# Kernel tuning notes

Hardware: AMD Instinct MI355X
Metric: run time of the kernel (lower is better)

The kernel has to match this reference:

```python
import jax, jax.numpy as jnp
import numpy as np

WINDOW = 5
D_CONV = 4
HEADDIM = 64
NGROUPS = 1
EPS = 1e-5


def _silu(x):
    return x * jax.nn.sigmoid(x)


def _causal_dwconv(x, w, b):
    # x: (B, L, C), w: (C, K), b: (C,) -- depthwise causal conv along L
    K = w.shape[1]
    L = x.shape[1]
    xp = jnp.pad(x, ((0, 0), (K - 1, 0), (0, 0)))
    y = b
    for k in range(K):
        y = y + xp[:, k:k + L, :] * w[:, k]
    return y


def _mamba2_layer(x, in_w, cw, cb, dtb, A_log, Dh, nw, ow):
    # x: (B, L, dim). Mamba2 mixer (mamba_ssm defaults: ngroups=1, rmsnorm gated, no proj bias)
    B, L, _ = x.shape
    d_inner = nw.shape[0]
    nheads = dtb.shape[0]
    p = d_inner // nheads
    conv_dim = cw.shape[0]
    n = (conv_dim - d_inner) // 2  # d_state
    zxbcdt = x @ in_w.T  # (B, L, 2*d_inner + 2*n + nheads)
    z, xBC, dt = jnp.split(zxbcdt, [d_inner, d_inner + conv_dim], axis=-1)
    dt = jax.nn.softplus(dt + dtb)  # (B, L, h)
    xBC = _silu(_causal_dwconv(xBC, cw, cb))
    xh, Bm, Cm = jnp.split(xBC, [d_inner, d_inner + n], axis=-1)
    xh = xh.reshape(B, L, nheads, p)
    A = -jnp.exp(A_log)  # (h,)

    def step(h, inp):
        dt_t, x_t, B_t, C_t = inp  # (B,h), (B,h,p), (B,n), (B,n)
        decay = jnp.exp(dt_t * A)  # (B,h)
        h = h * decay[..., None, None] + (dt_t[..., None] * x_t)[..., None] * B_t[:, None, None, :]
        y = jnp.einsum('bhpn,bn->bhp', h, C_t)
        return h, y

    h0 = jnp.zeros((B, nheads, p, n), x.dtype)
    _, ys = jax.lax.scan(step, h0, (dt.transpose(1, 0, 2), xh.transpose(1, 0, 2, 3),
                                    Bm.transpose(1, 0, 2), Cm.transpose(1, 0, 2)))
    y = ys.transpose(1, 0, 2, 3) + Dh[None, None, :, None] * xh  # (B, L, h, p)
    y = y.reshape(B, L, d_inner)
    # gated RMSNorm (norm_before_gate=False): gate then normalize
    y = y * _silu(z)
    y = y * jax.lax.rsqrt(jnp.mean(y * y, axis=-1, keepdims=True) + EPS) * nw
    return y @ ow.T


def setup_inputs() -> dict:
    key = jax.random.key(0)
    ks = iter(jax.random.split(key, 24))
    B, T, C = 8, 2048, 3
    dim, depth, d_state, expand = 128, 4, 64, 2
    d_inner = expand * dim
    nheads = d_inner // HEADDIM
    conv_dim = d_inner + 2 * NGROUPS * d_state
    d_in_proj = 2 * d_inner + 2 * NGROUPS * d_state + nheads
    nrm = lambda shp, s=1.0: jax.random.normal(next(ks), shp, jnp.float32) * s
    return {
        'x': nrm((B, T, C)),
        'mlp_w1': nrm((128, C * WINDOW), 0.2), 'mlp_b1': jnp.zeros((128,), jnp.float32),
        'mlp_w2': nrm((dim, 128), 0.1), 'mlp_b2': jnp.zeros((dim,), jnp.float32),
        'cls_token': nrm((1, 1, dim)),
        'in_proj_w': nrm((depth, d_in_proj, dim), 0.05),
        'conv_w': nrm((depth, conv_dim, D_CONV), 0.3),
        'conv_b': jnp.zeros((depth, conv_dim), jnp.float32),
        'dt_bias': nrm((depth, nheads), 0.5),
        'A_log': jnp.log(jax.random.uniform(next(ks), (depth, nheads), jnp.float32, 1.0, 16.0)),
        'Dh': jnp.ones((depth, nheads), jnp.float32),
        'norm_w': jnp.ones((depth, d_inner), jnp.float32),
        'out_proj_w': nrm((depth, dim, d_inner), 0.05),
        'ln_w': jnp.ones((dim,), jnp.float32), 'ln_b': jnp.zeros((dim,), jnp.float32),
        'head_w': nrm((1, dim), 0.1), 'head_b': jnp.zeros((1,), jnp.float32),
    }


def reference(x, mlp_w1, mlp_b1, mlp_w2, mlp_b2, cls_token, in_proj_w, conv_w, conv_b,
              dt_bias, A_log, Dh, norm_w, out_proj_w, ln_w, ln_b, head_w, head_b):
    B, T, C = x.shape
    L = T - WINDOW + 1
    # Unfold + rearrange 'b (c w) l -> b l (w c)' == sliding windows flattened (window outer, channel inner)
    tok = jnp.stack([x[:, k:k + L, :] for k in range(WINDOW)], axis=2).reshape(B, L, WINDOW * C)
    h = jax.nn.gelu(tok @ mlp_w1.T + mlp_b1, approximate=False) @ mlp_w2.T + mlp_b2
    dim = h.shape[-1]
    h = jnp.concatenate([h, jnp.broadcast_to(cls_token, (B, 1, dim))], axis=1)
    for i in range(in_proj_w.shape[0]):
        h = _mamba2_layer(h, in_proj_w[i], conv_w[i], conv_b[i], dt_bias[i],
                          A_log[i], Dh[i], norm_w[i], out_proj_w[i])
    cls = h[:, -1]
    mu = jnp.mean(cls, axis=-1, keepdims=True)
    var = jnp.mean((cls - mu) ** 2, axis=-1, keepdims=True)
    cls_n = (cls - mu) * jax.lax.rsqrt(var + 1e-5) * ln_w + ln_b
    out = (cls_n @ head_w.T + head_b)[:, 0]
    return out, h
```

## Files before the change

### kernel.cpp

```cpp
#include <hip/hip_runtime.h>
#include <math.h>

#define BATCH 8
#define TSEQ 2048
#define CIN 3
#define WIN 5
#define LSEQ 2044
#define LH 2045
#define LHP 2048
#define DIM 128
#define DEPTH 4
#define DIN 256
#define NH 4
#define PDIM 64
#define NSTATE 64
#define CONVD 384
#define DPROJ 644
#define NJT 41
#define QC 64
#define NCH 32
#define LDS2 68
#define LDSY 268
#define LDSH 140
#define FTR 32
#define OTOK 32

typedef __attribute__((ext_vector_type(8))) short bf16x8;
typedef __attribute__((ext_vector_type(4))) float f32x4;
union Frag8 { bf16x8 v; uint2 u[2]; };

__device__ __forceinline__ float sigmoidf_(float x){ return 1.f/(1.f+__expf(-x)); }
__device__ __forceinline__ float siluf_(float x){ return x*sigmoidf_(x); }
__device__ __forceinline__ unsigned short f2bf(float f){
  unsigned int u = __float_as_uint(f);
  return (unsigned short)((u + 0x7FFFu + ((u >> 16) & 1u)) >> 16);
}
__device__ __forceinline__ float bf2f(unsigned short u){
  return __uint_as_float(((unsigned int)u) << 16);
}
__device__ __forceinline__ unsigned int pack2(float a, float b){
  return (unsigned int)f2bf(a) | ((unsigned int)f2bf(b) << 16);
}
__device__ __forceinline__ unsigned int pack2lo(float a, float b){
  float ra = a - bf2f(f2bf(a)), rb = b - bf2f(f2bf(b));
  return (unsigned int)f2bf(ra) | ((unsigned int)f2bf(rb) << 16);
}
__device__ __forceinline__ bf16x8 ldfrag(const unsigned short* base, int off){
  Frag8 f;
  f.u[0] = *(const uint2*)(base + off);
  f.u[1] = *(const uint2*)(base + off + 4);
  return f.v;
}

__global__ void __launch_bounds__(256) k_cast_all(
    const float* __restrict__ w, const float* __restrict__ ow,
    const float* __restrict__ cls,
    unsigned short* __restrict__ wH, unsigned short* __restrict__ wL,
    unsigned short* __restrict__ oH, unsigned short* __restrict__ oL,
    unsigned short* __restrict__ hH, unsigned short* __restrict__ hL) {
  int blk = blockIdx.x;
  if (blk < 164) {
    int gid = blk*256 + threadIdx.x;
    int lane = gid & 63;
    int kb = (gid >> 6) & 3;
    int jt = (gid >> 8) % NJT;
    int ly = gid / (NJT*4*64);
    int m = lane & 15, q = lane >> 4;
    int j = jt*16 + m;
    int k = kb*32 + q*8;
    unsigned short hi[8], lo[8];
    if (j < DPROJ) {
      const float* src = w + ((size_t)ly*DPROJ + j)*DIM + k;
#pragma unroll
      for (int i = 0; i < 8; ++i) {
        float v = src[i];
        hi[i] = f2bf(v);
        lo[i] = f2bf(v - bf2f(hi[i]));
      }
    } else {
#pragma unroll
      for (int i = 0; i < 8; ++i) { hi[i] = 0; lo[i] = 0; }
    }
    size_t dst = (size_t)gid*8;
    *(uint4*)(wH + dst) = *(const uint4*)hi;
    *(uint4*)(wL + dst) = *(const uint4*)lo;
  } else if (blk < 228) {
    int gid = (blk - 164)*256 + threadIdx.x;
    int lane = gid & 63;
    int kb = (gid >> 6) & 7;
    int jt = (gid >> 9) & 7;
    int ly = gid >> 12;
    int m = lane & 15, q = lane >> 4;
    int j = jt*16 + m;
    int k = kb*32 + q*8;
    const float* src = ow + ((size_t)ly*DIM + j)*DIN + k;
    unsigned short hi[8], lo[8];
#pragma unroll
    for (int i = 0; i < 8; ++i) {
      float v = src[i];
      hi[i] = f2bf(v);
      lo[i] = f2bf(v - bf2f(hi[i]));
    }
    size_t dst = (size_t)gid*8;
    *(uint4*)(oH + dst) = *(const uint4*)hi;
    *(uint4*)(oL + dst) = *(const uint4*)lo;
  } else {
    int t = threadIdx.x;
    if (t < DIM) {
      float cv = cls[t];
      unsigned short hi = f2bf(cv);
      unsigned short lo = f2bf(cv - bf2f(hi));
      for (int b = 0; b < BATCH; ++b) {
        hH[((size_t)b*LHP + LSEQ)*DIM + t] = hi;
        hL[((size_t)b*LHP + LSEQ)*DIM + t] = lo;
      }
    }
  }
}

__global__ void __launch_bounds__(512) k_front(
    const float* __restrict__ x, const float* __restrict__ w1,
    const float* __restrict__ b1, const float* __restrict__ w2,
    const float* __restrict__ b2,
    unsigned short* __restrict__ hH, unsigned short* __restrict__ hL) {
  int t = threadIdx.x;
  int b = blockIdx.x >> 6;
  int c0 = (blockIdx.x & 63) * FTR;
  __shared__ float xs[(FTR+4)*CIN];
  __shared__ float w1s[DIM*17];
  __shared__ __align__(16) float h1s[FTR][DIM];
  __shared__ float part[FTR][DIM][2];
  for (int i = t; i < (FTR+4)*CIN; i += 512) {
    int row = c0 + i/3, ch = i - (i/3)*3;
    xs[i] = (row < TSEQ) ? x[(size_t)b*TSEQ*CIN + (size_t)row*CIN + ch] : 0.f;
  }
  for (int i = t; i < DIM*15; i += 512) {
    int j = i/15, k = i - j*15;
    w1s[j*17+k] = w1[i];
  }
  __syncthreads();
  {
    int j = t & 127, rh = t >> 7;
    float bias = b1[j];
    const float* wr = &w1s[j*17];
    for (int r = rh*8; r < rh*8+8; ++r) {
      float a = bias;
#pragma unroll
      for (int k = 0; k < 15; ++k) a += xs[r*3+k]*wr[k];
      h1s[r][j] = 0.5f*a*(1.f + erff(a*0.70710678118654752f));
    }
  }
  __syncthreads();
  {
    int j = t & 127, z = t >> 7;
    int hf = z & 1, rh2 = z >> 1;
    float4 wv[16];
    const float4* w2r = (const float4*)(w2 + (size_t)j*DIM + hf*64);
#pragma unroll
    for (int k4 = 0; k4 < 16; ++k4) wv[k4] = w2r[k4];
#pragma unroll 2
    for (int r = rh2*16; r < rh2*16+16; ++r) {
      const float4* hr = (const float4*)&h1s[r][hf*64];
      float acc = 0.f;
#pragma unroll
      for (int k4 = 0; k4 < 16; ++k4) {
        float4 hv = hr[k4];
        acc += wv[k4].x*hv.x + wv[k4].y*hv.y + wv[k4].z*hv.z + wv[k4].w*hv.w;
      }
      part[r][j][hf] = acc;
    }
  }
  __syncthreads();
  {
    int c = t & 127, rh = t >> 7;
    float bias = b2[c];
    for (int r = rh*8; r < rh*8+8; ++r) {
      int l = c0 + r;
      if (l < LSEQ) {
        float val = part[r][c][0] + part[r][c][1] + bias;
        unsigned short hi = f2bf(val);
        hH[((size_t)b*LHP + l)*DIM + c] = hi;
        hL[((size_t)b*LHP + l)*DIM + c] = f2bf(val - bf2f(hi));
      }
    }
  }
}

__global__ void __launch_bounds__(256) k_inproj_mfma(
    const unsigned short* __restrict__ hH, const unsigned short* __restrict__ hL,
    const unsigned short* __restrict__ wH, const unsigned short* __restrict__ wL,
    const float* __restrict__ dtb, float* __restrict__ zx) {
  int b = blockIdx.x >> 6;
  int r = blockIdx.x & 63;
  int lb = r >> 1, jh = r & 1;
  int wv = threadIdx.x >> 6, lane = threadIdx.x & 63;
  int l0 = lb*64 + wv*16;
  int m = lane & 15, q = lane >> 4;
  size_t hoff = ((size_t)b*LHP + (l0 + m))*DIM + q*8;
  bf16x8 ah[4], al[4];
#pragma unroll
  for (int kb = 0; kb < 4; ++kb) {
    ah[kb] = *(const bf16x8*)(hH + hoff + kb*32);
    al[kb] = *(const bf16x8*)(hL + hoff + kb*32);
  }
  int jt0 = jh ? 21 : 0, jtn = jh ? NJT : 21;
#pragma unroll 2
  for (int jt = jt0; jt < jtn; ++jt) {
    size_t woff = (((size_t)jt*4)*64 + lane)*8;
    bf16x8 bh[4], bl[4];
#pragma unroll
    for (int kb = 0; kb < 4; ++kb) {
      bh[kb] = *(const bf16x8*)(wH + woff + (size_t)kb*64*8);
      bl[kb] = *(const bf16x8*)(wL + woff + (size_t)kb*64*8);
    }
    f32x4 acc = {0.f, 0.f, 0.f, 0.f};
#pragma unroll
    for (int kb = 0; kb < 4; ++kb)
      acc = __builtin_amdgcn_mfma_f32_16x16x32_bf16(al[kb], bh[kb], acc, 0, 0, 0);
#pragma unroll
    for (int kb = 0; kb < 4; ++kb)
      acc = __builtin_amdgcn_mfma_f32_16x16x32_bf16(ah[kb], bl[kb], acc, 0, 0, 0);
#pragma unroll
    for (int kb = 0; kb < 4; ++kb)
      acc = __builtin_amdgcn_mfma_f32_16x16x32_bf16(ah[kb], bh[kb], acc, 0, 0, 0);
    int jj = jt*16 + m;
    if (jj < DPROJ) {
      bool isdt = (jj >= 640);
      float bias = isdt ? dtb[jj - 640] : 0.f;
#pragma unroll
      for (int rr = 0; rr < 4; ++rr) {
        int tok = l0 + q*4 + rr;
        if (tok < LH) {
          float v = acc[rr];
          if (isdt) { v += bias; v = (v > 20.f) ? v : log1pf(__expf(v)); }
          zx[((size_t)b*LH + tok)*DPROJ + jj] = v;
        }
      }
    }
  }
}

__global__ void k_conv(const float* __restrict__ zx, const float* __restrict__ cw,
                       const float* __restrict__ cb, float* __restrict__ xbc) {
  size_t idx = (size_t)blockIdx.x*blockDim.x + threadIdx.x;
  const size_t total = (size_t)BATCH*LH*(CONVD/4);
  if (idx >= total) return;
  int c4 = (int)(idx % (CONVD/4)) * 4;
  size_t bl = idx / (CONVD/4);
  int l = (int)(bl % LH); int b = (int)(bl / LH);
  float4 w0 = *(const float4*)(cw + (c4+0)*4);
  float4 w1 = *(const float4*)(cw + (c4+1)*4);
  float4 w2 = *(const float4*)(cw + (c4+2)*4);
  float4 w3 = *(const float4*)(cw + (c4+3)*4);
  float4 a = *(const float4*)(cb + c4);
#pragma unroll
  for (int k = 0; k < 4; ++k) {
    int tin = l - 3 + k;
    if (tin >= 0) {
      float4 v = *(const float4*)(zx + ((size_t)b*LH + tin)*DPROJ + DIN + c4);
      a.x += v.x * ((const float*)&w0)[k];
      a.y += v.y * ((const float*)&w1)[k];
      a.z += v.z * ((const float*)&w2)[k];
      a.w += v.w * ((const float*)&w3)[k];
    }
  }
  float4 o;
  o.x = siluf_(a.x); o.y = siluf_(a.y); o.z = siluf_(a.z); o.w = siluf_(a.w);
  *(float4*)(xbc + ((size_t)b*LH + l)*CONVD + c4) = o;
}

__global__ void __launch_bounds__(256, 4) k_chunk_state(
    const float* __restrict__ zx, const float* __restrict__ xbc,
    const float* __restrict__ A_log, float* __restrict__ G, float* __restrict__ dec) {
  int blk = blockIdx.x;
  int c = blk & (NCH-1), hd = (blk >> 5) & 3, b = blk >> 7;
  int t0 = c*QC;
  int tid = threadIdx.x;
  int wv = tid >> 6, lane = tid & 63;
  int m = lane & 15, q = lane >> 4;
  float A = -__expf(A_log[hd]);
  __shared__ __align__(16) unsigned short BcH[QC*LDS2], BcL[QC*LDS2];
  __shared__ __align__(16) unsigned short XtH[QC*LDS2], XtL[QC*LDS2];
  __shared__ float coef[QC];
  float dtv = 0.f;
  if (tid < 64) {
    int tg = t0 + tid;
    dtv = (tg < LH) ? zx[((size_t)b*LH + tg)*DPROJ + 640 + hd] : 0.f;
  }
  float pb[16], px[16];
#pragma unroll
  for (int it = 0; it < 8; ++it) {
    int i = tid + it*256;
    int n = i & 63, s2 = (i >> 6)*2;
    int tg0 = t0 + s2, tg1 = tg0 + 1;
    float b0 = 0.f, b1 = 0.f, x0 = 0.f, x1 = 0.f;
    if (tg0 < LH) {
      size_t row = ((size_t)b*LH + tg0)*CONVD;
      b0 = xbc[row + DIN + n];
      x0 = xbc[row + hd*PDIM + n];
    }
    if (tg1 < LH) {
      size_t row = ((size_t)b*LH + tg1)*CONVD;
      b1 = xbc[row + DIN + n];
      x1 = xbc[row + hd*PDIM + n];
    }
    pb[it*2] = b0; pb[it*2+1] = b1; px[it*2] = x0; px[it*2+1] = x1;
  }
  if (tid < 64) {
    float s = dtv;
#pragma unroll
    for (int off = 1; off < 64; off <<= 1) {
      float u = __shfl_up(s, off);
      if (tid >= off) s += u;
    }
    float cq = __shfl(s, 63);
    coef[tid] = __expf(A*(cq - s)) * dtv;
    if (tid == 63) dec[blk] = __expf(A * s);
  }
  __syncthreads();
#pragma unroll
  for (int it = 0; it < 8; ++it) {
    int i = tid + it*256;
    int n = i & 63, s2 = (i >> 6)*2;
    float c0_ = coef[s2], c1_ = coef[s2+1];
    float b0 = pb[it*2]*c0_, b1 = pb[it*2+1]*c1_;
    float x0 = px[it*2],     x1 = px[it*2+1];
    int o = n*LDS2 + s2;
    *(unsigned int*)(BcH + o) = pack2(b0, b1);
    *(unsigned int*)(BcL + o) = pack2lo(b0, b1);
    *(unsigned int*)(XtH + o) = pack2(x0, x1);
    *(unsigned int*)(XtL + o) = pack2lo(x0, x1);
  }
  __syncthreads();
  bf16x8 ah[2], al[2];
#pragma unroll
  for (int kc = 0; kc < 2; ++kc) {
    int off = (wv*16 + m)*LDS2 + kc*32 + q*8;
    ah[kc] = ldfrag(BcH, off);
    al[kc] = ldfrag(BcL, off);
  }
#pragma unroll
  for (int nt = 0; nt < 4; ++nt) {
    f32x4 acc = {0.f,0.f,0.f,0.f};
#pragma unroll
    for (int kc = 0; kc < 2; ++kc) {
      int off = (nt*16 + m)*LDS2 + kc*32 + q*8;
      bf16x8 xh = ldfrag(XtH, off), xl = ldfrag(XtL, off);
      acc = __builtin_amdgcn_mfma_f32_16x16x32_bf16(al[kc], xh, acc, 0, 0, 0);
      acc = __builtin_amdgcn_mfma_f32_16x16x32_bf16(ah[kc], xl, acc, 0, 0, 0);
      acc = __builtin_amdgcn_mfma_f32_16x16x32_bf16(ah[kc], xh, acc, 0, 0, 0);
    }
    int p = nt*16 + m;
#pragma unroll
    for (int r = 0; r < 4; ++r) {
      int n = wv*16 + q*4 + r;
      G[(size_t)blk*4096 + n*64 + p] = acc[r];
    }
  }
}

__global__ void __launch_bounds__(256) k_combine(
    const float* __restrict__ G, const float* __restrict__ dec, float* __restrict__ Hin) {
  int bh = blockIdx.x >> 2, esp = blockIdx.x & 3;
  int e = esp*1024 + threadIdx.x*4;
  size_t base0 = (size_t)bh*NCH*4096 + e;
  float4 gq[4]; float dq[4];
#pragma unroll
  for (int k = 0; k < 4; ++k) {
    gq[k] = *(const float4*)(G + base0 + (size_t)k*4096);
    dq[k] = dec[bh*NCH + k];
  }
  float4 H = make_float4(0.f,0.f,0.f,0.f);
#pragma unroll 4
  for (int c = 0; c < NCH; ++c) {
    int slot = c & 3;
    float4 g = gq[slot]; float d = dq[slot];
    if (c + 4 < NCH) {
      gq[slot] = *(const float4*)(G + base0 + (size_t)(c+4)*4096);
      dq[slot] = dec[bh*NCH + c + 4];
    }
    *(float4*)(Hin + base0 + (size_t)c*4096) = H;
    H.x = H.x*d + g.x; H.y = H.y*d + g.y; H.z = H.z*d + g.z; H.w = H.w*d + g.w;
  }
}

__global__ void __launch_bounds__(256, 4) k_chunk_out(
    const float* __restrict__ zx, const float* __restrict__ xbc,
    const float* __restrict__ A_log, const float* __restrict__ Hin,
    float* __restrict__ y) {
  int blk = blockIdx.x;
  int c = blk & (NCH-1), hd = (blk >> 5) & 3, b = blk >> 7;
  int t0 = c*QC;
  int tid = threadIdx.x;
  int wv = tid >> 6, lane = tid & 63;
  int m = lane & 15, q = lane >> 4;
  float A = -__expf(A_log[hd]);
  __shared__ __align__(16) unsigned short P0H[QC*LDS2], P0L[QC*LDS2];
  __shared__ __align__(16) unsigned short P1H[QC*LDS2], P1L[QC*LDS2];
  __shared__ float cum[QC], dts[QC], pref[QC];
  float dtv = 0.f;
  if (tid < 64) {
    int tg = t0 + tid;
    dtv = (tg < LH) ? zx[((size_t)b*LH + tg)*DPROJ + 640 + hd] : 0.f;
  }
  float pbv[16], pcv[16];
#pragma unroll
  for (int it = 0; it < 8; ++it) {
    int i = tid + it*256;
    int s = i >> 5, j2 = (i & 31)*2;
    int tg = t0 + s;
    float b0 = 0.f, b1 = 0.f, c0_ = 0.f, c1_ = 0.f;
    if (tg < LH) {
      size_t row = ((size_t)b*LH + tg)*CONVD;
      float2 bv = *(const float2*)(xbc + row + DIN + j2);
      float2 cv = *(const float2*)(xbc + row + DIN + NSTATE + j2);
      b0 = bv.x; b1 = bv.y; c0_ = cv.x; c1_ = cv.y;
    }
    pbv[it*2] = b0; pbv[it*2+1] = b1; pcv[it*2] = c0_; pcv[it*2+1] = c1_;
  }
  size_t hbase = (size_t)blk*4096;
  float hv[16];
#pragma unroll
  for (int it = 0; it < 8; ++it) {
    int i = tid + it*256;
    int p = i & 63, n2 = (i >> 6)*2;
    hv[it*2]   = Hin[hbase + (size_t)n2*64 + p];
    hv[it*2+1] = Hin[hbase + (size_t)(n2+1)*64 + p];
  }
  if (tid < 64) {
    float s = dtv;
#pragma unroll
    for (int off = 1; off < 64; off <<= 1) {
      float u = __shfl_up(s, off);
      if (tid >= off) s += u;
    }
    dts[tid] = dtv; cum[tid] = s; pref[tid] = __expf(A*s);
  }
#pragma unroll
  for (int it = 0; it < 8; ++it) {
    int i = tid + it*256;
    int s = i >> 5, j2 = (i & 31)*2;
    int o = s*LDS2 + j2;
    *(unsigned int*)(P1H + o) = pack2(pbv[it*2], pbv[it*2+1]);
    *(unsigned int*)(P1L + o) = pack2lo(pbv[it*2], pbv[it*2+1]);
    *(unsigned int*)(P0H + o) = pack2(pcv[it*2], pcv[it*2+1]);
    *(unsigned int*)(P0L + o) = pack2lo(pcv[it*2], pcv[it*2+1]);
  }
  __syncthreads();
  bf16x8 ch[2], cl[2];
#pragma unroll
  for (int kc = 0; kc < 2; ++kc) {
    int off = (wv*16 + m)*LDS2 + kc*32 + q*8;
    ch[kc] = ldfrag(P0H, off);
    cl[kc] = ldfrag(P0L, off);
  }
  f32x4 sacc[4];
#pragma unroll
  for (int nt = 0; nt < 4; ++nt) {
    f32x4 a1 = {0.f,0.f,0.f,0.f};
#pragma unroll
    for (int kc = 0; kc < 2; ++kc) {
      int off = (nt*16 + m)*LDS2 + kc*32 + q*8;
      bf16x8 bh = ldfrag(P1H, off), bl = ldfrag(P1L, off);
      a1 = __builtin_amdgcn_mfma_f32_16x16x32_bf16(cl[kc], bh, a1, 0, 0, 0);
      a1 = __builtin_amdgcn_mfma_f32_16x16x32_bf16(ch[kc], bl, a1, 0, 0, 0);
      a1 = __builtin_amdgcn_mfma_f32_16x16x32_bf16(ch[kc], bh, a1, 0, 0, 0);
    }
    sacc[nt] = a1;
  }
  __syncthreads();
  float xv[16];
#pragma unroll
  for (int it = 0; it < 8; ++it) {
    int i = tid + it*256;
    int p = i & 63, s2 = (i >> 6)*2;
    int tg = t0 + s2;
    xv[it*2]   = (tg < LH)   ? xbc[((size_t)b*LH + tg)*CONVD + hd*PDIM + p]   : 0.f;
    xv[it*2+1] = (tg+1 < LH) ? xbc[((size_t)b*LH + tg+1)*CONVD + hd*PDIM + p] : 0.f;
  }
#pragma unroll
  for (int nt = 0; nt < 4; ++nt) {
    int s = nt*16 + m;
#pragma unroll
    for (int r = 0; r < 4; ++r) {
      int t = wv*16 + q*4 + r;
      float mv = 0.f;
      if (s <= t) mv = sacc[nt][r] * __expf(A*(cum[t] - cum[s])) * dts[s];
      unsigned short hi = f2bf(mv);
      P0H[t*LDS2 + s] = hi;
      P0L[t*LDS2 + s] = f2bf(mv - bf2f(hi));
    }
  }
#pragma unroll
  for (int it = 0; it < 8; ++it) {
    int i = tid + it*256;
    int p = i & 63, n2 = (i >> 6)*2;
    int o = p*LDS2 + n2;
    *(unsigned int*)(P1H + o) = pack2(hv[it*2], hv[it*2+1]);
    *(unsigned int*)(P1L + o) = pack2lo(hv[it*2], hv[it*2+1]);
  }
  __syncthreads();
  f32x4 y2a[4];
#pragma unroll
  for (int nt = 0; nt < 4; ++nt) {
    f32x4 a2 = {0.f,0.f,0.f,0.f};
#pragma unroll
    for (int kc = 0; kc < 2; ++kc) {
      int off = (nt*16 + m)*LDS2 + kc*32 + q*8;
      bf16x8 th = ldfrag(P1H, off), tl = ldfrag(P1L, off);
      a2 = __builtin_amdgcn_mfma_f32_16x16x32_bf16(cl[kc], th, a2, 0, 0, 0);
      a2 = __builtin_amdgcn_mfma_f32_16x16x32_bf16(ch[kc], tl, a2, 0, 0, 0);
      a2 = __builtin_amdgcn_mfma_f32_16x16x32_bf16(ch[kc], th, a2, 0, 0, 0);
    }
    y2a[nt] = a2;
  }
  bf16x8 mh[2], ml[2];
#pragma unroll
  for (int kc = 0; kc < 2; ++kc) {
    int off = (wv*16 + m)*LDS2 + kc*32 + q*8;
    mh[kc] = ldfrag(P0H, off);
    ml[kc] = ldfrag(P0L, off);
  }
  __syncthreads();
#pragma unroll
  for (int it = 0; it < 8; ++it) {
    int i = tid + it*256;
    int p = i & 63, s2 = (i >> 6)*2;
    int o = p*LDS2 + s2;
    *(unsigned int*)(P1H + o) = pack2(xv[it*2], xv[it*2+1]);
    *(unsigned int*)(P1L + o) = pack2lo(xv[it*2], xv[it*2+1]);
  }
  __syncthreads();
#pragma unroll
  for (int nt = 0; nt < 4; ++nt) {
    f32x4 a1 = {0.f,0.f,0.f,0.f};
#pragma unroll
    for (int kc = 0; kc < 2; ++kc) {
      int off = (nt*16 + m)*LDS2 + kc*32 + q*8;
      bf16x8 th = ldfrag(P1H, off), tl = ldfrag(P1L, off);
      a1 = __builtin_amdgcn_mfma_f32_16x16x32_bf16(ml[kc], th, a1, 0, 0, 0);
      a1 = __builtin_amdgcn_mfma_f32_16x16x32_bf16(mh[kc], tl, a1, 0, 0, 0);
      a1 = __builtin_amdgcn_mfma_f32_16x16x32_bf16(mh[kc], th, a1, 0, 0, 0);
    }
    int p = nt*16 + m;
#pragma unroll
    for (int r = 0; r < 4; ++r) {
      int t = wv*16 + q*4 + r, tg = t0 + t;
      if (tg < LH)
        y[((size_t)b*LH + tg)*DIN + hd*PDIM + p] = a1[r] + pref[t]*y2a[nt][r];
    }
  }
}

__global__ void __launch_bounds__(512, 4) k_out_fused(
    const float* __restrict__ y, const float* __restrict__ xbc,
    float* __restrict__ zx, const float* __restrict__ Dh,
    const float* __restrict__ nw, const unsigned short* __restrict__ oH,
    const unsigned short* __restrict__ oL,
    const unsigned short* __restrict__ wH, const unsigned short* __restrict__ wL,
    const float* __restrict__ dtb, float* __restrict__ hout, int doProj) {
  int b = blockIdx.x >> 6;
  int l0 = (blockIdx.x & 63) * OTOK;
  int t = threadIdx.x;
  __shared__ __align__(16) unsigned short yH[OTOK*LDSY], yL[OTOK*LDSY];
  __shared__ __align__(16) unsigned short hsH[OTOK*LDSH], hsL[OTOK*LDSH];
  __shared__ float red[OTOK][4];
  __shared__ float rs[OTOK];
  int wave = t >> 6, lane = t & 63;
  bf16x8 pwh[4], pwl[4];
#pragma unroll
  for (int kb = 0; kb < 4; ++kb) {
    size_t woff = (((size_t)wave*8 + kb)*64 + lane)*8;
    pwh[kb] = *(const bf16x8*)(oH + woff);
    pwl[kb] = *(const bf16x8*)(oL + woff);
  }
  int c = t & 255;
  int rh = t >> 8;
  int r0 = rh*16;
  int hd = c >> 6;
  float dcoef = Dh[hd];
  float nwc = nw[c];
  float v[16];
#pragma unroll
  for (int r = 0; r < 16; ++r) {
    int l = l0 + r0 + r;
    float val = 0.f;
    if (l < LH) {
      size_t row = (size_t)b*LH + l;
      float ys = y[row*DIN + c];
      float xh = xbc[row*CONVD + c];
      float z  = zx[row*DPROJ + c];
      val = (ys + dcoef*xh) * siluf_(z);
    }
    v[r] = val;
  }
  int qw = wave & 3;
#pragma unroll
  for (int r = 0; r < 16; ++r) {
    float sq = v[r]*v[r];
    for (int off = 32; off > 0; off >>= 1) sq += __shfl_down(sq, off);
    if (lane == 0) red[r0 + r][qw] = sq;
  }
  __syncthreads();
  if (t < OTOK) {
    float sm = red[t][0]+red[t][1]+red[t][2]+red[t][3];
    rs[t] = rsqrtf(sm/(float)DIN + 1e-5f);
  }
  __syncthreads();
#pragma unroll
  for (int r = 0; r < 16; ++r) {
    float val = v[r] * rs[r0 + r] * nwc;
    unsigned short hi = f2bf(val);
    yH[(r0 + r)*LDSY + c] = hi;
    yL[(r0 + r)*LDSY + c] = f2bf(val - bf2f(hi));
  }
  __syncthreads();
  int m = lane & 15, q = lane >> 4;
  {
    int jt = wave;
    f32x4 acc0 = {0.f,0.f,0.f,0.f}, acc1 = {0.f,0.f,0.f,0.f};
#pragma unroll
    for (int kb = 0; kb < 8; ++kb) {
      bf16x8 bh, bl;
      if (kb < 4) { bh = pwh[kb]; bl = pwl[kb]; }
      else {
        size_t woff = (((size_t)jt*8 + kb)*64 + lane)*8;
        bh = *(const bf16x8*)(oH + woff);
        bl = *(const bf16x8*)(oL + woff);
      }
      int o0 = m*LDSY + kb*32 + q*8;
      int o1 = (16 + m)*LDSY + kb*32 + q*8;
      bf16x8 a0h = ldfrag(yH, o0), a0l = ldfrag(yL, o0);
      bf16x8 a1h = ldfrag(yH, o1), a1l = ldfrag(yL, o1);
      acc0 = __builtin_amdgcn_mfma_f32_16x16x32_bf16(a0l, bh, acc0, 0, 0, 0);
      acc0 = __builtin_amdgcn_mfma_f32_16x16x32_bf16(a0h, bl, acc0, 0, 0, 0);
      acc0 = __builtin_amdgcn_mfma_f32_16x16x32_bf16(a0h, bh, acc0, 0, 0, 0);
      acc1 = __builtin_amdgcn_mfma_f32_16x16x32_bf16(a1l, bh, acc1, 0, 0, 0);
      acc1 = __builtin_amdgcn_mfma_f32_16x16x32_bf16(a1h, bl, acc1, 0, 0, 0);
      acc1 = __builtin_amdgcn_mfma_f32_16x16x32_bf16(a1h, bh, acc1, 0, 0, 0);
    }
    int j = jt*16 + m;
#pragma unroll
    for (int r = 0; r < 4; ++r) {
      int rr = q*4 + r;
      float val = acc0[r];
      unsigned short hi = f2bf(val);
// ... 64 lines not shown
  int b = blockIdx.x; int t = threadIdx.x;
  __shared__ float red[2];
  int wave = t >> 6, lane = t & 63;
  float v = h[((size_t)b*LH + LSEQ)*DIM + t];
  float s = v;
  for (int off = 32; off > 0; off >>= 1) s += __shfl_down(s, off);
  if (lane == 0) red[wave] = s;
  __syncthreads();
  float mean = (red[0]+red[1]) / (float)DIM;
  __syncthreads();
  float d = v - mean; float sq = d*d;
  for (int off = 32; off > 0; off >>= 1) sq += __shfl_down(sq, off);
  if (lane == 0) red[wave] = sq;
  __syncthreads();
  float var = (red[0]+red[1]) / (float)DIM;
  float cn = d*rsqrtf(var + 1e-5f)*lnw[t] + lnb[t];
  float dot = cn*hw[t];
  __syncthreads();
  for (int off = 32; off > 0; off >>= 1) dot += __shfl_down(dot, off);
  if (lane == 0) red[wave] = dot;
  __syncthreads();
  if (t == 0) out[b] = red[0]+red[1] + hb[0];
}

extern "C" void kernel_launch(void* const* d_in, const int* in_sizes, int n_in,
                              void* d_out, int out_size, void* d_ws, size_t ws_size,
                              hipStream_t stream) {
  const float* x     = (const float*)d_in[0];
  const float* w1    = (const float*)d_in[1];
  const float* b1    = (const float*)d_in[2];
  const float* w2    = (const float*)d_in[3];
  const float* b2    = (const float*)d_in[4];
  const float* cls   = (const float*)d_in[5];
  const float* inw   = (const float*)d_in[6];
  const float* cw    = (const float*)d_in[7];
  const float* cb    = (const float*)d_in[8];
  const float* dtb   = (const float*)d_in[9];
  const float* Alog  = (const float*)d_in[10];
  const float* Dh    = (const float*)d_in[11];
  const float* nw    = (const float*)d_in[12];
  const float* ow    = (const float*)d_in[13];
  const float* lnw   = (const float*)d_in[14];
  const float* lnb   = (const float*)d_in[15];
  const float* hw    = (const float*)d_in[16];
  const float* hb    = (const float*)d_in[17];

  float* ws   = (float*)d_ws;
  float* zx   = ws;
  float* xbc  = zx + (size_t)BATCH*LH*DPROJ;
  float* ybuf = xbc + (size_t)BATCH*LH*CONVD;
  float* G    = ybuf;
  float* Hin  = ybuf + 4194304;
  float* dec  = Hin  + 4194304;
  unsigned short* hH = (unsigned short*)(dec + 1024);
  unsigned short* hL = hH + (size_t)BATCH*LHP*DIM;
  unsigned short* wH = hL + (size_t)BATCH*LHP*DIM;
  unsigned short* wL = wH + (size_t)DEPTH*NJT*4*64*8;
  unsigned short* oH = wL + (size_t)DEPTH*NJT*4*64*8;
  unsigned short* oL = oH + (size_t)DEPTH*8*8*64*8;

  float* hout = (float*)d_out + 8;

  k_cast_all<<<229, 256, 0, stream>>>(inw, ow, cls, wH, wL, oH, oL, hH, hL);

  k_front<<<BATCH*64, 512, 0, stream>>>(x, w1, b1, w2, b2, hH, hL);
  k_inproj_mfma<<<BATCH*64, 256, 0, stream>>>(hH, hL, wH, wL, dtb, zx);

  for (int i = 0; i < DEPTH; ++i) {
    int doProj = (i < DEPTH-1) ? 1 : 0;
    int nxt = doProj ? (i+1) : 0;
    k_conv<<<(int)(((long)BATCH*LH*(CONVD/4) + 255)/256), 256, 0, stream>>>(
        zx, cw + (size_t)i*CONVD*4, cb + (size_t)i*CONVD, xbc);
    k_chunk_state<<<BATCH*NH*NCH, 256, 0, stream>>>(zx, xbc, Alog + i*NH, G, dec);
    k_combine<<<BATCH*NH*4, 256, 0, stream>>>(G, dec, Hin);
    k_chunk_out<<<BATCH*NH*NCH, 256, 0, stream>>>(zx, xbc, Alog + i*NH, Hin, ybuf);
    k_out_fused<<<BATCH*64, 512, 0, stream>>>(
        ybuf, xbc, zx, Dh + i*NH, nw + (size_t)i*DIN,
        oH + (size_t)i*8*8*64*8, oL + (size_t)i*8*8*64*8,
        wH + (size_t)nxt*NJT*4*64*8, wL + (size_t)nxt*NJT*4*64*8,
        dtb + nxt*NH, hout, doProj);
  }

  k_head<<<BATCH, 128, 0, stream>>>(hout, lnw, lnb, hw, hb, (float*)d_out);
}
```

Before: 510.4 us.

## Fuse causal depthwise conv into chunk-state, chunk-out and output kernels

Removes the standalone conv+SiLU kernel and its xbc intermediate buffer, recomputing the depthwise causal conv and SiLU on the fly from zx inside k_chunk_state, k_chunk_out and k_out_fused. This saves one launch per layer and the write and re-read of the conv output. In exchange the conv is recomputed redundantly, since B/C columns are evaluated by every head's blocks. Each thread now walks sequentially over tokens for one column, so the zx reads are strided by row and less coalesced.

```diff
diff --git a/kernel.cpp b/kernel.cpp
--- a/kernel.cpp
+++ b/kernel.cpp
@@ -240,38 +240,10 @@
   }
 }
 
-__global__ void k_conv(const float* __restrict__ zx, const float* __restrict__ cw,
-                       const float* __restrict__ cb, float* __restrict__ xbc) {
-  size_t idx = (size_t)blockIdx.x*blockDim.x + threadIdx.x;
-  const size_t total = (size_t)BATCH*LH*(CONVD/4);
-  if (idx >= total) return;
-  int c4 = (int)(idx % (CONVD/4)) * 4;
-  size_t bl = idx / (CONVD/4);
-  int l = (int)(bl % LH); int b = (int)(bl / LH);
-  float4 w0 = *(const float4*)(cw + (c4+0)*4);
-  float4 w1 = *(const float4*)(cw + (c4+1)*4);
-  float4 w2 = *(const float4*)(cw + (c4+2)*4);
-  float4 w3 = *(const float4*)(cw + (c4+3)*4);
-  float4 a = *(const float4*)(cb + c4);
-#pragma unroll
-  for (int k = 0; k < 4; ++k) {
-    int tin = l - 3 + k;
-    if (tin >= 0) {
-      float4 v = *(const float4*)(zx + ((size_t)b*LH + tin)*DPROJ + DIN + c4);
-      a.x += v.x * ((const float*)&w0)[k];
-      a.y += v.y * ((const float*)&w1)[k];
-      a.z += v.z * ((const float*)&w2)[k];
-      a.w += v.w * ((const float*)&w3)[k];
-    }
-  }
-  float4 o;
-  o.x = siluf_(a.x); o.y = siluf_(a.y); o.z = siluf_(a.z); o.w = siluf_(a.w);
-  *(float4*)(xbc + ((size_t)b*LH + l)*CONVD + c4) = o;
-}
-
 __global__ void __launch_bounds__(256, 4) k_chunk_state(
-    const float* __restrict__ zx, const float* __restrict__ xbc,
-    const float* __restrict__ A_log, float* __restrict__ G, float* __restrict__ dec) {
+    const float* __restrict__ zx, const float* __restrict__ cw,
+    const float* __restrict__ cb, const float* __restrict__ A_log,
+    float* __restrict__ G, float* __restrict__ dec) {
   int blk = blockIdx.x;
   int c = blk & (NCH-1), hd = (blk >> 5) & 3, b = blk >> 7;
   int t0 = c*QC;
@@ -282,31 +254,9 @@
   __shared__ __align__(16) unsigned short BcH[QC*LDS2], BcL[QC*LDS2];
   __shared__ __align__(16) unsigned short XtH[QC*LDS2], XtL[QC*LDS2];
   __shared__ float coef[QC];
-  float dtv = 0.f;
   if (tid < 64) {
     int tg = t0 + tid;
-    dtv = (tg < LH) ? zx[((size_t)b*LH + tg)*DPROJ + 640 + hd] : 0.f;
-  }
-  float pb[16], px[16];
-#pragma unroll
-  for (int it = 0; it < 8; ++it) {
-    int i = tid + it*256;
-    int n = i & 63, s2 = (i >> 6)*2;
-    int tg0 = t0 + s2, tg1 = tg0 + 1;
-    float b0 = 0.f, b1 = 0.f, x0 = 0.f, x1 = 0.f;
-    if (tg0 < LH) {
-      size_t row = ((size_t)b*LH + tg0)*CONVD;
-      b0 = xbc[row + DIN + n];
-      x0 = xbc[row + hd*PDIM + n];
-    }
-    if (tg1 < LH) {
-      size_t row = ((size_t)b*LH + tg1)*CONVD;
-      b1 = xbc[row + DIN + n];
-      x1 = xbc[row + hd*PDIM + n];
-    }
-    pb[it*2] = b0; pb[it*2+1] = b1; px[it*2] = x0; px[it*2+1] = x1;
-  }
-  if (tid < 64) {
+    float dtv = (tg < LH) ? zx[((size_t)b*LH + tg)*DPROJ + 640 + hd] : 0.f;
     float s = dtv;
 #pragma unroll
     for (int off = 1; off < 64; off <<= 1) {
@@ -318,18 +268,41 @@
     if (tid == 63) dec[blk] = __expf(A * s);
   }
   __syncthreads();
-#pragma unroll
-  for (int it = 0; it < 8; ++it) {
-    int i = tid + it*256;
-    int n = i & 63, s2 = (i >> 6)*2;
-    float c0_ = coef[s2], c1_ = coef[s2+1];
-    float b0 = pb[it*2]*c0_, b1 = pb[it*2+1]*c1_;
-    float x0 = px[it*2],     x1 = px[it*2+1];
-    int o = n*LDS2 + s2;
-    *(unsigned int*)(BcH + o) = pack2(b0, b1);
-    *(unsigned int*)(BcL + o) = pack2lo(b0, b1);
-    *(unsigned int*)(XtH + o) = pack2(x0, x1);
-    *(unsigned int*)(XtL + o) = pack2lo(x0, x1);
+  {
+    int chIdx = tid & 127, half = tid >> 7;
+    bool isB = (chIdx >= 64);
+    int n = chIdx & 63;
+    int col = isB ? (512 + n) : (256 + hd*PDIM + n);
+    int ch = col - 256;
+    const float4 w = *(const float4*)(cw + ch*4);
+    float bias = cb[ch];
+    unsigned short* dstH = isB ? BcH : XtH;
+    unsigned short* dstL = isB ? BcL : XtL;
+    int s0 = half*32;
+    float x3, x2, x1;
+    {
+      int t3 = t0 + s0 - 3, t2_ = t0 + s0 - 2, t1_ = t0 + s0 - 1;
+      x3 = (t3 >= 0 && t3 < LH) ? zx[((size_t)b*LH + t3)*DPROJ + col] : 0.f;
+      x2 = (t2_ >= 0 && t2_ < LH) ? zx[((size_t)b*LH + t2_)*DPROJ + col] : 0.f;
+      x1 = (t1_ >= 0 && t1_ < LH) ? zx[((size_t)b*LH + t1_)*DPROJ + col] : 0.f;
+    }
+    float prev = 0.f;
+#pragma unroll
+    for (int i = 0; i < 32; ++i) {
+      int s = s0 + i;
+      int tg = t0 + s;
+      float x0 = (tg < LH) ? zx[((size_t)b*LH + tg)*DPROJ + col] : 0.f;
+      float a = bias;
+      a += x3*w.x; a += x2*w.y; a += x1*w.z; a += x0*w.w;
+      float out = (tg < LH) ? siluf_(a) : 0.f;
+      if (isB) out *= coef[s];
+      if (i & 1) {
+        int o = n*LDS2 + (s - 1);
+        *(unsigned int*)(dstH + o) = pack2(prev, out);
+        *(unsigned int*)(dstL + o) = pack2lo(prev, out);
+      } else prev = out;
+      x3 = x2; x2 = x1; x1 = x0;
+    }
   }
   __syncthreads();
   bf16x8 ah[2], al[2];
@@ -385,9 +358,9 @@
 }
 
 __global__ void __launch_bounds__(256, 4) k_chunk_out(
-    const float* __restrict__ zx, const float* __restrict__ xbc,
-    const float* __restrict__ A_log, const float* __restrict__ Hin,
-    float* __restrict__ y) {
+    const float* __restrict__ zx, const float* __restrict__ cw,
+    const float* __restrict__ cb, const float* __restrict__ A_log,
+    const float* __restrict__ Hin, float* __restrict__ y) {
   int blk = blockIdx.x;
   int c = blk & (NCH-1), hd = (blk >> 5) & 3, b = blk >> 7;
   int t0 = c*QC;
@@ -403,21 +376,6 @@
     int tg = t0 + tid;
     dtv = (tg < LH) ? zx[((size_t)b*LH + tg)*DPROJ + 640 + hd] : 0.f;
   }
-  float pbv[16], pcv[16];
-#pragma unroll
-  for (int it = 0; it < 8; ++it) {
-    int i = tid + it*256;
-    int s = i >> 5, j2 = (i & 31)*2;
-    int tg = t0 + s;
-    float b0 = 0.f, b1 = 0.f, c0_ = 0.f, c1_ = 0.f;
-    if (tg < LH) {
-      size_t row = ((size_t)b*LH + tg)*CONVD;
-      float2 bv = *(const float2*)(xbc + row + DIN + j2);
-      float2 cv = *(const float2*)(xbc + row + DIN + NSTATE + j2);
-      b0 = bv.x; b1 = bv.y; c0_ = cv.x; c1_ = cv.y;
-    }
-    pbv[it*2] = b0; pbv[it*2+1] = b1; pcv[it*2] = c0_; pcv[it*2+1] = c1_;
-  }
   size_t hbase = (size_t)blk*4096;
   float hv[16];
 #pragma unroll
@@ -427,6 +385,63 @@
     hv[it*2]   = Hin[hbase + (size_t)n2*64 + p];
     hv[it*2+1] = Hin[hbase + (size_t)(n2+1)*64 + p];
   }
+  {
+    int chIdx = tid & 127, half = tid >> 7;
+    bool isC = (chIdx >= 64);
+    int n = chIdx & 63;
+    int col = (isC ? 576 : 512) + n;
+    int ch = col - 256;
+    const float4 w = *(const float4*)(cw + ch*4);
+    float bias = cb[ch];
+    unsigned short* dstH = isC ? P0H : P1H;
+    unsigned short* dstL = isC ? P0L : P1L;
+    int s0 = half*32;
+    float x3, x2, x1;
+    {
+      int t3 = t0 + s0 - 3, t2_ = t0 + s0 - 2, t1_ = t0 + s0 - 1;
+      x3 = (t3 >= 0 && t3 < LH) ? zx[((size_t)b*LH + t3)*DPROJ + col] : 0.f;
+      x2 = (t2_ >= 0 && t2_ < LH) ? zx[((size_t)b*LH + t2_)*DPROJ + col] : 0.f;
+      x1 = (t1_ >= 0 && t1_ < LH) ? zx[((size_t)b*LH + t1_)*DPROJ + col] : 0.f;
+    }
+#pragma unroll
+    for (int i = 0; i < 32; ++i) {
+      int s = s0 + i;
+      int tg = t0 + s;
+      float x0 = (tg < LH) ? zx[((size_t)b*LH + tg)*DPROJ + col] : 0.f;
+      float a = bias;
+      a += x3*w.x; a += x2*w.y; a += x1*w.z; a += x0*w.w;
+      float out = (tg < LH) ? siluf_(a) : 0.f;
+      unsigned short hi = f2bf(out);
+      dstH[s*LDS2 + n] = hi;
+      dstL[s*LDS2 + n] = f2bf(out - bf2f(hi));
+      x3 = x2; x2 = x1; x1 = x0;
+    }
+  }
+  float xr[16];
+  {
+    int p = tid & 63, qt = tid >> 6;
+    int col = 256 + hd*PDIM + p;
+    int ch = col - 256;
+    const float4 w = *(const float4*)(cw + ch*4);
+    float bias = cb[ch];
+    int s0 = qt*16;
+    float x3, x2, x1;
+    {
+      int t3 = t0 + s0 - 3, t2_ = t0 + s0 - 2, t1_ = t0 + s0 - 1;
+      x3 = (t3 >= 0 && t3 < LH) ? zx[((size_t)b*LH + t3)*DPROJ + col] : 0.f;
+      x2 = (t2_ >= 0 && t2_ < LH) ? zx[((size_t)b*LH + t2_)*DPROJ + col] : 0.f;
+      x1 = (t1_ >= 0 && t1_ < LH) ? zx[((size_t)b*LH + t1_)*DPROJ + col] : 0.f;
+    }
+#pragma unroll
+    for (int i = 0; i < 16; ++i) {
+      int tg = t0 + s0 + i;
+      float x0 = (tg < LH) ? zx[((size_t)b*LH + tg)*DPROJ + col] : 0.f;
+      float a = bias;
+      a += x3*w.x; a += x2*w.y; a += x1*w.z; a += x0*w.w;
+      xr[i] = (tg < LH) ? siluf_(a) : 0.f;
+      x3 = x2; x2 = x1; x1 = x0;
+    }
+  }
   if (tid < 64) {
     float s = dtv;
 #pragma unroll
@@ -436,23 +451,13 @@
     }
     dts[tid] = dtv; cum[tid] = s; pref[tid] = __expf(A*s);
   }
-#pragma unroll
-  for (int it = 0; it < 8; ++it) {
-    int i = tid + it*256;
-    int s = i >> 5, j2 = (i & 31)*2;
-    int o = s*LDS2 + j2;
-    *(unsigned int*)(P1H + o) = pack2(pbv[it*2], pbv[it*2+1]);
-    *(unsigned int*)(P1L + o) = pack2lo(pbv[it*2], pbv[it*2+1]);
-    *(unsigned int*)(P0H + o) = pack2(pcv[it*2], pcv[it*2+1]);
-    *(unsigned int*)(P0L + o) = pack2lo(pcv[it*2], pcv[it*2+1]);
-  }
-  __syncthreads();
-  bf16x8 ch[2], cl[2];
+  __syncthreads();
+  bf16x8 ch_[2], cl_[2];
 #pragma unroll
   for (int kc = 0; kc < 2; ++kc) {
     int off = (wv*16 + m)*LDS2 + kc*32 + q*8;
-    ch[kc] = ldfrag(P0H, off);
-    cl[kc] = ldfrag(P0L, off);
+    ch_[kc] = ldfrag(P0H, off);
+    cl_[kc] = ldfrag(P0L, off);
   }
   f32x4 sacc[4];
 #pragma unroll
@@ -462,22 +467,13 @@
     for (int kc = 0; kc < 2; ++kc) {
       int off = (nt*16 + m)*LDS2 + kc*32 + q*8;
       bf16x8 bh = ldfrag(P1H, off), bl = ldfrag(P1L, off);
-      a1 = __builtin_amdgcn_mfma_f32_16x16x32_bf16(cl[kc], bh, a1, 0, 0, 0);
-      a1 = __builtin_amdgcn_mfma_f32_16x16x32_bf16(ch[kc], bl, a1, 0, 0, 0);
-      a1 = __builtin_amdgcn_mfma_f32_16x16x32_bf16(ch[kc], bh, a1, 0, 0, 0);
+      a1 = __builtin_amdgcn_mfma_f32_16x16x32_bf16(cl_[kc], bh, a1, 0, 0, 0);
+      a1 = __builtin_amdgcn_mfma_f32_16x16x32_bf16(ch_[kc], bl, a1, 0, 0, 0);
+      a1 = __builtin_amdgcn_mfma_f32_16x16x32_bf16(ch_[kc], bh, a1, 0, 0, 0);
     }
     sacc[nt] = a1;
   }
   __syncthreads();
-  float xv[16];
-#pragma unroll
-  for (int it = 0; it < 8; ++it) {
-    int i = tid + it*256;
-    int p = i & 63, s2 = (i >> 6)*2;
-    int tg = t0 + s2;
-    xv[it*2]   = (tg < LH)   ? xbc[((size_t)b*LH + tg)*CONVD + hd*PDIM + p]   : 0.f;
-    xv[it*2+1] = (tg+1 < LH) ? xbc[((size_t)b*LH + tg+1)*CONVD + hd*PDIM + p] : 0.f;
-  }
 #pragma unroll
   for (int nt = 0; nt < 4; ++nt) {
     int s = nt*16 + m;
@@ -508,9 +504,9 @@
     for (int kc = 0; kc < 2; ++kc) {
       int off = (nt*16 + m)*LDS2 + kc*32 + q*8;
       bf16x8 th = ldfrag(P1H, off), tl = ldfrag(P1L, off);
-      a2 = __builtin_amdgcn_mfma_f32_16x16x32_bf16(cl[kc], th, a2, 0, 0, 0);
-      a2 = __builtin_amdgcn_mfma_f32_16x16x32_bf16(ch[kc], tl, a2, 0, 0, 0);
-      a2 = __builtin_amdgcn_mfma_f32_16x16x32_bf16(ch[kc], th, a2, 0, 0, 0);
+      a2 = __builtin_amdgcn_mfma_f32_16x16x32_bf16(cl_[kc], th, a2, 0, 0, 0);
+      a2 = __builtin_amdgcn_mfma_f32_16x16x32_bf16(ch_[kc], tl, a2, 0, 0, 0);
+      a2 = __builtin_amdgcn_mfma_f32_16x16x32_bf16(ch_[kc], th, a2, 0, 0, 0);
     }
     y2a[nt] = a2;
   }
@@ -522,13 +518,15 @@
     ml[kc] = ldfrag(P0L, off);
   }
   __syncthreads();
-#pragma unroll
-  for (int it = 0; it < 8; ++it) {
-    int i = tid + it*256;
-    int p = i & 63, s2 = (i >> 6)*2;
-    int o = p*LDS2 + s2;
-    *(unsigned int*)(P1H + o) = pack2(xv[it*2], xv[it*2+1]);
-    *(unsigned int*)(P1L + o) = pack2lo(xv[it*2], xv[it*2+1]);
+  {
+    int p = tid & 63, qt = tid >> 6;
+    int s0 = qt*16;
+#pragma unroll
+    for (int j = 0; j < 8; ++j) {
+      int o = p*LDS2 + s0 + 2*j;
+      *(unsigned int*)(P1H + o) = pack2(xr[2*j], xr[2*j+1]);
+      *(unsigned int*)(P1L + o) = pack2lo(xr[2*j], xr[2*j+1]);
+    }
   }
   __syncthreads();
 #pragma unroll
@@ -553,10 +551,10 @@
 }
 
 __global__ void __launch_bounds__(512, 4) k_out_fused(
-    const float* __restrict__ y, const float* __restrict__ xbc,
-    float* __restrict__ zx, const float* __restrict__ Dh,
-    const float* __restrict__ nw, const unsigned short* __restrict__ oH,
-    const unsigned short* __restrict__ oL,
+    const float* __restrict__ y, float* __restrict__ zx,
+    const float* __restrict__ Dh, const float* __restrict__ nw,
+    const float* __restrict__ cw, const float* __restrict__ cb,
+    const unsigned short* __restrict__ oH, const unsigned short* __restrict__ oL,
     const unsigned short* __restrict__ wH, const unsigned short* __restrict__ wL,
     const float* __restrict__ dtb, float* __restrict__ hout, int doProj) {
   int b = blockIdx.x >> 6;
@@ -580,18 +578,33 @@
   int hd = c >> 6;
   float dcoef = Dh[hd];
   float nwc = nw[c];
+  const float4 wX = *(const float4*)(cw + c*4);
+  float cbX = cb[c];
   float v[16];
+  float x3, x2, x1;
+  {
+    int lst = l0 + r0;
+    int t3 = lst - 3, t2_ = lst - 2, t1_ = lst - 1;
+    x3 = (t3 >= 0) ? zx[((size_t)b*LH + t3)*DPROJ + 256 + c] : 0.f;
+    x2 = (t2_ >= 0) ? zx[((size_t)b*LH + t2_)*DPROJ + 256 + c] : 0.f;
+    x1 = (t1_ >= 0) ? zx[((size_t)b*LH + t1_)*DPROJ + 256 + c] : 0.f;
+  }
 #pragma unroll
   for (int r = 0; r < 16; ++r) {
     int l = l0 + r0 + r;
     float val = 0.f;
+    float x0v = 0.f;
     if (l < LH) {
       size_t row = (size_t)b*LH + l;
+      x0v = zx[row*DPROJ + 256 + c];
+      float a = cbX;
+      a += x3*wX.x; a += x2*wX.y; a += x1*wX.z; a += x0v*wX.w;
+      float xh = siluf_(a);
       float ys = y[row*DIN + c];
-      float xh = xbc[row*CONVD + c];
       float z  = zx[row*DPROJ + c];
       val = (ys + dcoef*xh) * siluf_(z);
     }
+    x3 = x2; x2 = x1; x1 = x0v;
     v[r] = val;
   }
   int qw = wave & 3;
@@ -768,6 +781,7 @@
   unsigned short* wL = wH + (size_t)DEPTH*NJT*4*64*8;
   unsigned short* oH = wL + (size_t)DEPTH*NJT*4*64*8;
   unsigned short* oL = oH + (size_t)DEPTH*8*8*64*8;
+  (void)xbc;
 
   float* hout = (float*)d_out + 8;
 
@@ -779,13 +793,13 @@
   for (int i = 0; i < DEPTH; ++i) {
     int doProj = (i < DEPTH-1) ? 1 : 0;
     int nxt = doProj ? (i+1) : 0;
-    k_conv<<<(int)(((long)BATCH*LH*(CONVD/4) + 255)/256), 256, 0, stream>>>(
-        zx, cw + (size_t)i*CONVD*4, cb + (size_t)i*CONVD, xbc);
-    k_chunk_state<<<BATCH*NH*NCH, 256, 0, stream>>>(zx, xbc, Alog + i*NH, G, dec);
+    const float* cwi = cw + (size_t)i*CONVD*4;
+    const float* cbi = cb + (size_t)i*CONVD;
+    k_chunk_state<<<BATCH*NH*NCH, 256, 0, stream>>>(zx, cwi, cbi, Alog + i*NH, G, dec);
     k_combine<<<BATCH*NH*4, 256, 0, stream>>>(G, dec, Hin);
-    k_chunk_out<<<BATCH*NH*NCH, 256, 0, stream>>>(zx, xbc, Alog + i*NH, Hin, ybuf);
+    k_chunk_out<<<BATCH*NH*NCH, 256, 0, stream>>>(zx, cwi, cbi, Alog + i*NH, Hin, ybuf);
     k_out_fused<<<BATCH*64, 512, 0, stream>>>(
-        ybuf, xbc, zx, Dh + i*NH, nw + (size_t)i*DIN,
+        ybuf, zx, Dh + i*NH, nw + (size_t)i*DIN, cwi, cbi,
         oH + (size_t)i*8*8*64*8, oL + (size_t)i*8*8*64*8,
         wH + (size_t)nxt*NJT*4*64*8, wL + (size_t)nxt*NJT*4*64*8,
         dtb + nxt*NH, hout, doProj);
```

New measurement: 534.8 us. +4.8%, slower.

## Fuse front MLP with first-layer in_proj MFMA GEMM through shared memory

Applied to the files above, without the earlier changes.

The front token MLP kernel now also runs the first layer's in_proj GEMM. It writes the split bf16 hi/lo activations into an aliased shared-memory pool instead of global hH/hL buffers, and each of 8 waves computes a strided set of output column tiles for the block's 32 tokens. The cls token row is now written inside this kernel, so the cast kernel loses that job. This removes one launch and the global round trip of the activations. In exchange, each block reloads every weight tile, and the GEMM tile is 32 tokens rather than 64 per block.

```diff
diff --git a/kernel.cpp b/kernel.cpp
--- a/kernel.cpp
+++ b/kernel.cpp
@@ -54,10 +54,8 @@
 
 __global__ void __launch_bounds__(256) k_cast_all(
     const float* __restrict__ w, const float* __restrict__ ow,
-    const float* __restrict__ cls,
     unsigned short* __restrict__ wH, unsigned short* __restrict__ wL,
-    unsigned short* __restrict__ oH, unsigned short* __restrict__ oL,
-    unsigned short* __restrict__ hH, unsigned short* __restrict__ hL) {
+    unsigned short* __restrict__ oH, unsigned short* __restrict__ oL) {
   int blk = blockIdx.x;
   if (blk < 164) {
     int gid = blk*256 + threadIdx.x;
@@ -84,7 +82,7 @@
     size_t dst = (size_t)gid*8;
     *(uint4*)(wH + dst) = *(const uint4*)hi;
     *(uint4*)(wL + dst) = *(const uint4*)lo;
-  } else if (blk < 228) {
+  } else {
     int gid = (blk - 164)*256 + threadIdx.x;
     int lane = gid & 63;
     int kb = (gid >> 6) & 7;
@@ -104,32 +102,25 @@
     size_t dst = (size_t)gid*8;
     *(uint4*)(oH + dst) = *(const uint4*)hi;
     *(uint4*)(oL + dst) = *(const uint4*)lo;
-  } else {
-    int t = threadIdx.x;
-    if (t < DIM) {
-      float cv = cls[t];
-      unsigned short hi = f2bf(cv);
-      unsigned short lo = f2bf(cv - bf2f(hi));
-      for (int b = 0; b < BATCH; ++b) {
-        hH[((size_t)b*LHP + LSEQ)*DIM + t] = hi;
-        hL[((size_t)b*LHP + LSEQ)*DIM + t] = lo;
-      }
-    }
-  }
-}
-
-__global__ void __launch_bounds__(512) k_front(
+  }
+}
+
+__global__ void __launch_bounds__(512) k_front_proj(
     const float* __restrict__ x, const float* __restrict__ w1,
     const float* __restrict__ b1, const float* __restrict__ w2,
-    const float* __restrict__ b2,
-    unsigned short* __restrict__ hH, unsigned short* __restrict__ hL) {
+    const float* __restrict__ b2, const float* __restrict__ cls,
+    const unsigned short* __restrict__ wH, const unsigned short* __restrict__ wL,
+    const float* __restrict__ dtb, float* __restrict__ zx) {
   int t = threadIdx.x;
   int b = blockIdx.x >> 6;
   int c0 = (blockIdx.x & 63) * FTR;
-  __shared__ float xs[(FTR+4)*CIN];
-  __shared__ float w1s[DIM*17];
-  __shared__ __align__(16) float h1s[FTR][DIM];
-  __shared__ float part[FTR][DIM][2];
+  __shared__ __align__(16) float pool[108 + 2176 + 4096 + 8192];
+  float* xs   = pool;
+  float* w1s  = pool + 108;
+  float* h1s  = pool + 108 + 2176;
+  float* part = pool + 108 + 2176 + 4096;
+  unsigned short* hsH = (unsigned short*)pool;
+  unsigned short* hsL = hsH + 32*LDSH;
   for (int i = t; i < (FTR+4)*CIN; i += 512) {
     int row = c0 + i/3, ch = i - (i/3)*3;
     xs[i] = (row < TSEQ) ? x[(size_t)b*TSEQ*CIN + (size_t)row*CIN + ch] : 0.f;
@@ -147,7 +138,7 @@
       float a = bias;
 #pragma unroll
       for (int k = 0; k < 15; ++k) a += xs[r*3+k]*wr[k];
-      h1s[r][j] = 0.5f*a*(1.f + erff(a*0.70710678118654752f));
+      h1s[r*128 + j] = 0.5f*a*(1.f + erff(a*0.70710678118654752f));
     }
   }
   __syncthreads();
@@ -160,14 +151,14 @@
     for (int k4 = 0; k4 < 16; ++k4) wv[k4] = w2r[k4];
 #pragma unroll 2
     for (int r = rh2*16; r < rh2*16+16; ++r) {
-      const float4* hr = (const float4*)&h1s[r][hf*64];
+      const float4* hr = (const float4*)&h1s[r*128 + hf*64];
       float acc = 0.f;
 #pragma unroll
       for (int k4 = 0; k4 < 16; ++k4) {
         float4 hv = hr[k4];
         acc += wv[k4].x*hv.x + wv[k4].y*hv.y + wv[k4].z*hv.z + wv[k4].w*hv.w;
       }
-      part[r][j][hf] = acc;
+      part[(r*128 + j)*2 + hf] = acc;
     }
   }
   __syncthreads();
@@ -176,36 +167,20 @@
     float bias = b2[c];
     for (int r = rh*8; r < rh*8+8; ++r) {
       int l = c0 + r;
-      if (l < LSEQ) {
-        float val = part[r][c][0] + part[r][c][1] + bias;
-        unsigned short hi = f2bf(val);
-        hH[((size_t)b*LHP + l)*DIM + c] = hi;
-        hL[((size_t)b*LHP + l)*DIM + c] = f2bf(val - bf2f(hi));
-      }
-    }
-  }
-}
-
-__global__ void __launch_bounds__(256) k_inproj_mfma(
-    const unsigned short* __restrict__ hH, const unsigned short* __restrict__ hL,
-    const unsigned short* __restrict__ wH, const unsigned short* __restrict__ wL,
-    const float* __restrict__ dtb, float* __restrict__ zx) {
-  int b = blockIdx.x >> 6;
-  int r = blockIdx.x & 63;
-  int lb = r >> 1, jh = r & 1;
-  int wv = threadIdx.x >> 6, lane = threadIdx.x & 63;
-  int l0 = lb*64 + wv*16;
+      float val;
+      if (l < LSEQ)       val = part[(r*128 + c)*2] + part[(r*128 + c)*2 + 1] + bias;
+      else if (l == LSEQ) val = cls[c];
+      else                val = 0.f;
+      unsigned short hi = f2bf(val);
+      hsH[r*LDSH + c] = hi;
+      hsL[r*LDSH + c] = f2bf(val - bf2f(hi));
+    }
+  }
+  __syncthreads();
+  int wave = t >> 6, lane = t & 63;
   int m = lane & 15, q = lane >> 4;
-  size_t hoff = ((size_t)b*LHP + (l0 + m))*DIM + q*8;
-  bf16x8 ah[4], al[4];
-#pragma unroll
-  for (int kb = 0; kb < 4; ++kb) {
-    ah[kb] = *(const bf16x8*)(hH + hoff + kb*32);
-    al[kb] = *(const bf16x8*)(hL + hoff + kb*32);
-  }
-  int jt0 = jh ? 21 : 0, jtn = jh ? NJT : 21;
 #pragma unroll 2
-  for (int jt = jt0; jt < jtn; ++jt) {
+  for (int jt = wave; jt < NJT; jt += 8) {
     size_t woff = (((size_t)jt*4)*64 + lane)*8;
     bf16x8 bh[4], bl[4];
 #pragma unroll
@@ -213,27 +188,37 @@
       bh[kb] = *(const bf16x8*)(wH + woff + (size_t)kb*64*8);
       bl[kb] = *(const bf16x8*)(wL + woff + (size_t)kb*64*8);
     }
-    f32x4 acc = {0.f, 0.f, 0.f, 0.f};
-#pragma unroll
-    for (int kb = 0; kb < 4; ++kb)
-      acc = __builtin_amdgcn_mfma_f32_16x16x32_bf16(al[kb], bh[kb], acc, 0, 0, 0);
-#pragma unroll
-    for (int kb = 0; kb < 4; ++kb)
-      acc = __builtin_amdgcn_mfma_f32_16x16x32_bf16(ah[kb], bl[kb], acc, 0, 0, 0);
-#pragma unroll
-    for (int kb = 0; kb < 4; ++kb)
-      acc = __builtin_amdgcn_mfma_f32_16x16x32_bf16(ah[kb], bh[kb], acc, 0, 0, 0);
+    f32x4 acc0 = {0.f, 0.f, 0.f, 0.f}, acc1 = {0.f, 0.f, 0.f, 0.f};
+#pragma unroll
+    for (int kb = 0; kb < 4; ++kb) {
+      int o0 = m*LDSH + kb*32 + q*8;
+      int o1 = (16 + m)*LDSH + kb*32 + q*8;
+      bf16x8 a0h = ldfrag(hsH, o0), a0l = ldfrag(hsL, o0);
+      bf16x8 a1h = ldfrag(hsH, o1), a1l = ldfrag(hsL, o1);
+      acc0 = __builtin_amdgcn_mfma_f32_16x16x32_bf16(a0l, bh[kb], acc0, 0, 0, 0);
+      acc0 = __builtin_amdgcn_mfma_f32_16x16x32_bf16(a0h, bl[kb], acc0, 0, 0, 0);
+      acc0 = __builtin_amdgcn_mfma_f32_16x16x32_bf16(a0h, bh[kb], acc0, 0, 0, 0);
+      acc1 = __builtin_amdgcn_mfma_f32_16x16x32_bf16(a1l, bh[kb], acc1, 0, 0, 0);
+      acc1 = __builtin_amdgcn_mfma_f32_16x16x32_bf16(a1h, bl[kb], acc1, 0, 0, 0);
+      acc1 = __builtin_amdgcn_mfma_f32_16x16x32_bf16(a1h, bh[kb], acc1, 0, 0, 0);
+    }
     int jj = jt*16 + m;
     if (jj < DPROJ) {
       bool isdt = (jj >= 640);
       float bias = isdt ? dtb[jj - 640] : 0.f;
 #pragma unroll
-      for (int rr = 0; rr < 4; ++rr) {
-        int tok = l0 + q*4 + rr;
+      for (int r = 0; r < 4; ++r) {
+        int tok = c0 + q*4 + r;
         if (tok < LH) {
-          float v = acc[rr];
-          if (isdt) { v += bias; v = (v > 20.f) ? v : log1pf(__expf(v)); }
-          zx[((size_t)b*LH + tok)*DPROJ + jj] = v;
+          float vv = acc0[r];
+          if (isdt) { vv += bias; vv = (vv > 20.f) ? vv : log1pf(__expf(vv)); }
+          zx[((size_t)b*LH + tok)*DPROJ + jj] = vv;
+        }
+        int tok1 = c0 + 16 + q*4 + r;
+        if (tok1 < LH) {
+          float vv = acc1[r];
+          if (isdt) { vv += bias; vv = (vv > 20.f) ? vv : log1pf(__expf(vv)); }
+          zx[((size_t)b*LH + tok1)*DPROJ + jj] = vv;
         }
       }
     }
@@ -762,19 +747,17 @@
   float* G    = ybuf;
   float* Hin  = ybuf + 4194304;
   float* dec  = Hin  + 4194304;
-  unsigned short* hH = (unsigned short*)(dec + 1024);
-  unsigned short* hL = hH + (size_t)BATCH*LHP*DIM;
-  unsigned short* wH = hL + (size_t)BATCH*LHP*DIM;
+  unsigned short* wH = (unsigned short*)(dec + 1024);
   unsigned short* wL = wH + (size_t)DEPTH*NJT*4*64*8;
   unsigned short* oH = wL + (size_t)DEPTH*NJT*4*64*8;
   unsigned short* oL = oH + (size_t)DEPTH*8*8*64*8;
 
   float* hout = (float*)d_out + 8;
 
-  k_cast_all<<<229, 256, 0, stream>>>(inw, ow, cls, wH, wL, oH, oL, hH, hL);
-
-  k_front<<<BATCH*64, 512, 0, stream>>>(x, w1, b1, w2, b2, hH, hL);
-  k_inproj_mfma<<<BATCH*64, 256, 0, stream>>>(hH, hL, wH, wL, dtb, zx);
+  k_cast_all<<<228, 256, 0, stream>>>(inw, ow, wH, wL, oH, oL);
+
+  k_front_proj<<<BATCH*64, 512, 0, stream>>>(x, w1, b1, w2, b2, cls,
+                                             wH, wL, dtb, zx);
 
   for (int i = 0; i < DEPTH; ++i) {
     int doProj = (i < DEPTH-1) ? 1 : 0;
```

Result: faster. 474.3 us (-7.1%).
